# Optimization experiments

Hardware: AMD Instinct MI355X
Metric: run time of the kernel (lower is better)

## Reference

```python
import jax, jax.numpy as jnp
import numpy as np

H, W = 96, 96          # output field size
D = 32                 # window_radius
WIN = 2 * D + 1        # 65
A, B, R = 15.0, 3.0, 1
EXP = 1.0 / (1 + R)    # exponent in the stable-like covariance


def _extract_patches(noise2d):
    wi = jnp.arange(WIN)
    rows = (jnp.arange(H)[:, None, None, None] + wi[None, None, :, None])
    cols = (jnp.arange(W)[None, :, None, None] + wi[None, None, None, :])
    patches = noise2d[rows, cols]
    return patches.reshape(H * W, WIN, WIN)


def _batch_autocorrelation(theta_vec):
    x = jnp.linspace(-D, D, WIN, dtype=jnp.float32)
    Xm, Ym = jnp.meshgrid(x, x, indexing='ij')
    c = jnp.cos(theta_vec)[:, None, None]
    s = jnp.sin(theta_vec)[:, None, None]
    a_part = (Xm[None] * c + Ym[None] * s) ** 2 / (A ** 2)
    b_part = (-Xm[None] * s + Ym[None] * c) ** 2 / (B ** 2)
    return jnp.exp(-(a_part + b_part) ** EXP)


def setup_inputs() -> dict:
    key = jax.random.key(0)
    k1, k2 = jax.random.split(key)
    angle_matrix = jax.random.uniform(k1, (H, W), dtype=jnp.float32) * (2.0 * np.pi)
    noise = jax.random.normal(k2, (1, 1, H + 2 * D, W + 2 * D), dtype=jnp.float32)
    return {"angle_matrix": angle_matrix, "noise": noise}


def reference(angle_matrix, noise):
    patches = _extract_patches(noise[0, 0])
    R_stack = _batch_autocorrelation(angle_matrix.reshape(-1))
    Wf = jnp.fft.fft2(patches)
    Rf = jnp.fft.fft2(jnp.fft.fftshift(R_stack, axes=(-2, -1)))
    G = jnp.sqrt(Rf + 1e-8)                                 # complex sqrt
    v = jnp.fft.ifft2(Wf * G).real
    mean = v.mean(axis=(1, 2), keepdims=True)
    std = v.std(axis=(1, 2), keepdims=True, ddof=1)         # torch unbiased std
    v = (v - mean) / (std + 1e-6)
    return v[:, D, D].reshape(H, W)
```

## Files before the change

kernel.cpp:

```cpp
#include <hip/hip_runtime.h>
#include <math.h>

#define HH 96
#define WW 96
#define NWIN 65
#define NZ 160
#define L33 33
#define PAD 36
#define NT 256
#define KT 3
#define NG 22

__global__ __launch_bounds__(NT)
void rowdft_kernel(const float* __restrict__ noise, float2* __restrict__ rd)
{
    __shared__ float row[NZ];
    __shared__ float2 tw[NWIN];
    const int tid = threadIdx.x;
    const int r = blockIdx.x;
    if (tid < NWIN) {
        double a = 6.283185307179586 * (double)tid / 65.0;
        tw[tid] = make_float2((float)cos(a), (float)sin(a));
    }
    if (tid < NZ) row[tid] = noise[r * NZ + tid];
    __syncthreads();

    for (int t = tid; t < 96 * 9; t += NT) {
        const int px = t / 9;
        const int g = t - 9 * px;
        const int l0 = 4 * g;
        float c0[4], c1[4], s0[4], s1[4], tc2[4], aC[4], aS[4];
        #pragma unroll
        for (int j = 0; j < 4; j++) {
            float2 w = tw[l0 + j];
            c0[j] = 1.f; s0[j] = 0.f;
            c1[j] = w.x; s1[j] = w.y;
            tc2[j] = 2.f * w.x;
            aC[j] = 0.f; aS[j] = 0.f;
        }
        for (int wx = 0; wx < NWIN; ++wx) {
            float v = row[px + wx];
            #pragma unroll
            for (int j = 0; j < 4; j++) {
                aC[j] = fmaf(v, c0[j], aC[j]);
                aS[j] = fmaf(v, s0[j], aS[j]);
                float cn = fmaf(tc2[j], c1[j], -c0[j]);
                float sn = fmaf(tc2[j], s1[j], -s0[j]);
                c0[j] = c1[j]; c1[j] = cn;
                s0[j] = s1[j]; s1[j] = sn;
            }
        }
        #pragma unroll
        for (int j = 0; j < 4; j++) {
            int l = l0 + j;
            if (l < L33) rd[(px * NZ + r) * L33 + l] = make_float2(aC[j], aS[j]);
        }
    }
}

__global__ __launch_bounds__(NT)
void fftma2_kernel(const float* __restrict__ angle,
                   const float2* __restrict__ rd,
                   float* __restrict__ out)
{
    __shared__ float2 tw[NWIN];
    __shared__ alignas(16) float  RbT[NWIN][PAD];
    __shared__ alignas(16) float  Tc[L33][PAD];
    __shared__ alignas(16) float  Ts[L33][PAD];
    __shared__ alignas(16) float2 Wst[NWIN][PAD];
    __shared__ float red[4][4];

    const int tid = threadIdx.x;
    const int p  = blockIdx.x;
    const int py = p / WW;
    const int px = p - py * WW;

    if (tid < NWIN) {
        double a = 6.283185307179586 * (double)tid / 65.0;
        tw[tid] = make_float2((float)cos(a), (float)sin(a));
    }

    const float th = angle[p];
    const float cth = cosf(th), sth = sinf(th);

    for (int e = tid; e < NWIN * PAD; e += NT) {
        int y = e / PAD, x = e - PAD * y;
        float v = 0.f;
        if (x < L33) {
            float X = (float)x;
            float Y = (float)(y <= 32 ? y : y - 65);
            float u =  X * cth + Y * sth;
            float w = -X * sth + Y * cth;
            float q = fmaf(u * (1.f / 225.f), u, w * (1.f / 9.f) * w);
            v = expf(-sqrtf(q));
        }
        RbT[y][x] = v;
    }
    {
        const float2* src = rd + (px * NZ + py) * L33;
        for (int e = tid; e < NWIN * PAD; e += NT) {
            int y = e / PAD, l = e - PAD * y;
            float2 v = make_float2(0.f, 0.f);
            if (l < L33) v = src[y * L33 + l];
            Wst[y][l] = v;
        }
    }
    __syncthreads();

    for (int t = tid; t < 9 * PAD; t += NT) {
        int xg = t / PAD, l = t - PAD * xg;
        int x0 = 4 * xg;
        float aC[4] = {0,0,0,0}, aS[4] = {0,0,0,0};
        float2 wl = tw[l];
        float cm = 1.f, sm = 0.f;
        float cc = wl.x, ss = wl.y;
        float t2 = 2.f * wl.x;
        for (int y = 0; y < NWIN; ++y) {
            const float4 rv = *(const float4*)&RbT[y][x0];
            aC[0] = fmaf(rv.x, cm, aC[0]); aS[0] = fmaf(rv.x, sm, aS[0]);
            aC[1] = fmaf(rv.y, cm, aC[1]); aS[1] = fmaf(rv.y, sm, aS[1]);
            aC[2] = fmaf(rv.z, cm, aC[2]); aS[2] = fmaf(rv.z, sm, aS[2]);
            aC[3] = fmaf(rv.w, cm, aC[3]); aS[3] = fmaf(rv.w, sm, aS[3]);
            float cn = fmaf(t2, cc, -cm);
            float sn = fmaf(t2, ss, -sm);
            cm = cc; sm = ss; cc = cn; ss = sn;
        }
        #pragma unroll
        for (int j = 0; j < 4; j++) {
            int x = x0 + j;
            if (x < L33) { Tc[x][l] = aC[j]; Ts[x][l] = aS[j]; }
        }
    }
    __syncthreads();

    float accA = 0.f, accP = 0.f, accC = 0.f, accV = 0.f;
    if (tid < NG * 9) {
        const int g  = tid / 9;
        const int lg = tid - 9 * g;
        const int l0 = 4 * lg;
        const int kb = KT * g;

        float stc2[KT], sc1[KT], ss1[KT];
        #pragma unroll
        for (int d = 0; d < KT; d++) {
            int kc = kb + d; if (kc >= NWIN) kc -= NWIN;
            float2 w = tw[kc];
            sc1[d] = w.x; ss1[d] = w.y; stc2[d] = 2.f * w.x;
        }

        const float4 tc0 = *(const float4*)&Tc[0][l0];
        float ac[KT][4];
        #pragma unroll
        for (int d = 0; d < KT; d++)
            #pragma unroll
            for (int j = 0; j < 4; j++) ac[d][j] = 0.f;
        {
            float cm[KT], sm[KT], cc[KT], ss[KT];
            #pragma unroll
            for (int d = 0; d < KT; d++) {
                cm[d] = 1.f; sm[d] = 0.f;
                cc[d] = sc1[d]; ss[d] = ss1[d];
            }
            for (int x = 1; x < L33; ++x) {
                const float4 c4 = *(const float4*)&Tc[x][l0];
                const float4 s4 = *(const float4*)&Ts[x][l0];
                #pragma unroll
                for (int d = 0; d < KT; d++) {
                    float cw = cc[d], sw = ss[d];
                    ac[d][0] = fmaf(c4.x, cw, ac[d][0]); ac[d][0] = fmaf(-s4.x, sw, ac[d][0]);
                    ac[d][1] = fmaf(c4.y, cw, ac[d][1]); ac[d][1] = fmaf(-s4.y, sw, ac[d][1]);
                    ac[d][2] = fmaf(c4.z, cw, ac[d][2]); ac[d][2] = fmaf(-s4.z, sw, ac[d][2]);
                    ac[d][3] = fmaf(c4.w, cw, ac[d][3]); ac[d][3] = fmaf(-s4.w, sw, ac[d][3]);
                    float cn = fmaf(stc2[d], cw, -cm[d]);
                    float sn = fmaf(stc2[d], sw, -sm[d]);
                    cm[d] = cw; sm[d] = sw; cc[d] = cn; ss[d] = sn;
                }
            }
        }

        float Wr[KT][4], Wi[KT][4];
        #pragma unroll
        for (int d = 0; d < KT; d++)
            #pragma unroll
            for (int j = 0; j < 4; j++) { Wr[d][j] = 0.f; Wi[d][j] = 0.f; }
        {
            float cm[KT], sm[KT], cc[KT], ss[KT];
            #pragma unroll
            for (int d = 0; d < KT; d++) {
                cm[d] = 1.f; sm[d] = 0.f;
                cc[d] = sc1[d]; ss[d] = ss1[d];
            }
            for (int y = 0; y < NWIN; ++y) {
                const float4 w01 = *(const float4*)&Wst[y][l0];
                const float4 w23 = *(const float4*)&Wst[y][l0 + 2];
                #pragma unroll
                for (int d = 0; d < KT; d++) {
                    float cw = cm[d], sw = sm[d];
                    Wr[d][0] = fmaf(w01.x, cw, Wr[d][0]); Wr[d][0] = fmaf(-w01.y, sw, Wr[d][0]);
                    Wi[d][0] = fmaf(-w01.x, sw, Wi[d][0]); Wi[d][0] = fmaf(-w01.y, cw, Wi[d][0]);
                    Wr[d][1] = fmaf(w01.z, cw, Wr[d][1]); Wr[d][1] = fmaf(-w01.w, sw, Wr[d][1]);
                    Wi[d][1] = fmaf(-w01.z, sw, Wi[d][1]); Wi[d][1] = fmaf(-w01.w, cw, Wi[d][1]);
                    Wr[d][2] = fmaf(w23.x, cw, Wr[d][2]); Wr[d][2] = fmaf(-w23.y, sw, Wr[d][2]);
                    Wi[d][2] = fmaf(-w23.x, sw, Wi[d][2]); Wi[d][2] = fmaf(-w23.y, cw, Wi[d][2]);
                    Wr[d][3] = fmaf(w23.z, cw, Wr[d][3]); Wr[d][3] = fmaf(-w23.w, sw, Wr[d][3]);
                    Wi[d][3] = fmaf(-w23.z, sw, Wi[d][3]); Wi[d][3] = fmaf(-w23.w, cw, Wi[d][3]);
                    float cn = fmaf(stc2[d], cc[d], -cw);
                    float sn = fmaf(stc2[d], ss[d], -sw);
                    cm[d] = cc[d]; sm[d] = ss[d]; cc[d] = cn; ss[d] = sn;
                }
            }
        }

        #pragma unroll
        for (int d = 0; d < KT; d++) {
            const int k = kb + d;
            if (k >= NWIN) continue;
            #pragma unroll
            for (int j = 0; j < 4; j++) {
                const int l = l0 + j;
                if (l > 32) continue;
                if (l == 0 && k > 32) continue;
                float wr = Wr[d][j], wi = Wi[d][j];
                float rho = fmaf(2.f, ac[d][j], (j==0)?tc0.x:(j==1)?tc0.y:(j==2)?tc0.z:tc0.w);
                int kl = k + l; if (kl >= NWIN) kl -= NWIN;
                float2 tkl = tw[kl];
                float zr = fmaf(rho, tkl.x, 1e-8f);
                float zi = rho * tkl.y;
                float rr = sqrtf(zr * zr + zi * zi);
                float Gr = sqrtf(fmaxf(0.5f * (rr + zr), 0.f));
                float Gm = sqrtf(fmaxf(0.5f * (rr - zr), 0.f));
                float Gi = (zi < 0.f) ? -Gm : Gm;
                float Fr = wr * Gr - wi * Gi;
                float Fi = wr * Gi + wi * Gr;
                if (k == 0 && l == 0) {
                    accA += Fr * Fr + Fi * Fi;
                    accP += Fr * Fr - Fi * Fi;
                    accC += Fr;
                    accV += Fr;
                } else {
                    float Gi2 = (zi == 0.f) ? Gi : -Gi;
                    float Fr2 = wr * Gr + wi * Gi2;
                    float Fi2 = wr * Gi2 - wi * Gr;
                    accA += Fr * Fr + Fi * Fi + Fr2 * Fr2 + Fi2 * Fi2;
                    accP += 2.f * (Fr * Fr2 - Fi * Fi2);
                    int m32 = (32 * (k + l)) % NWIN;
                    float2 t32 = tw[m32];
                    accC += Fr * t32.x - Fi * t32.y + Fr2 * t32.x + Fi2 * t32.y;
                }
            }
        }
    }

    #pragma unroll
    for (int off = 32; off > 0; off >>= 1) {
        accA += __shfl_down(accA, off);
        accP += __shfl_down(accP, off);
        accC += __shfl_down(accC, off);
        accV += __shfl_down(accV, off);
    }
    int wv = tid >> 6, ln = tid & 63;
    if (ln == 0) { red[wv][0] = accA; red[wv][1] = accP; red[wv][2] = accC; red[wv][3] = accV; }
    __syncthreads();
    if (tid == 0) {
        float A  = red[0][0] + red[1][0] + red[2][0] + red[3][0];
        float P  = red[0][1] + red[1][1] + red[2][1] + red[3][1];
        float Cs = red[0][2] + red[1][2] + red[2][2] + red[3][2];
        float V  = red[0][3] + red[1][3] + red[2][3] + red[3][3];
        const float Ntot = 4225.f;
        float mean = V / Ntot;
        float E2   = (P + A) * (0.5f / Ntot);
        float cen  = Cs / Ntot;
        float var  = (E2 - Ntot * mean * mean) / (Ntot - 1.f);
        float sd   = sqrtf(fmaxf(var, 0.f));
        out[p] = (cen - mean) / (sd + 1e-6f);
    }
}

extern "C" void kernel_launch(void* const* d_in, const int* in_sizes, int n_in,
                              void* d_out, int out_size, void* d_ws, size_t ws_size,
                              hipStream_t stream)
{
    (void)in_sizes; (void)n_in; (void)out_size; (void)ws_size;
    const float* angle = (const float*)d_in[0];
    const float* noise = (const float*)d_in[1];
    float* outp = (float*)d_out;
    float2* rd = (float2*)d_ws;

    rowdft_kernel<<<dim3(NZ), dim3(NT), 0, stream>>>(noise, rd);
    fftma2_kernel<<<dim3(HH * WW), dim3(NT), 0, stream>>>(angle, rd, outp);
}
```

Before: 874.5 us.

## Exploit k/65-k twiddle symmetry to halve column DFT work and shrink block

The column-direction DFTs now compute cosine and sine partial sums separately for frequency k, then build the results for both k and 65-k from them. Only k in 0..32 (17 groups of two) is computed, which roughly halves the recurrence and FMA work in the final stage. The block size drops from 256 to 192 threads so that fewer threads sit idle. The cost is that the earlier staging and DFT loops run with fewer threads per block, and more accumulators are held in registers.

```diff
diff --git a/kernel.cpp b/kernel.cpp
--- a/kernel.cpp
+++ b/kernel.cpp
@@ -7,11 +7,10 @@
 #define NZ 160
 #define L33 33
 #define PAD 36
-#define NT 256
-#define KT 3
-#define NG 22
-
-__global__ __launch_bounds__(NT)
+#define NT1 256
+#define NT2 192
+
+__global__ __launch_bounds__(NT1)
 void rowdft_kernel(const float* __restrict__ noise, float2* __restrict__ rd)
 {
     __shared__ float row[NZ];
@@ -25,7 +24,7 @@
     if (tid < NZ) row[tid] = noise[r * NZ + tid];
     __syncthreads();
 
-    for (int t = tid; t < 96 * 9; t += NT) {
+    for (int t = tid; t < 96 * 9; t += NT1) {
         const int px = t / 9;
         const int g = t - 9 * px;
         const int l0 = 4 * g;
@@ -58,7 +57,7 @@
     }
 }
 
-__global__ __launch_bounds__(NT)
+__global__ __launch_bounds__(NT2)
 void fftma2_kernel(const float* __restrict__ angle,
                    const float2* __restrict__ rd,
                    float* __restrict__ out)
@@ -68,7 +67,7 @@
     __shared__ alignas(16) float  Tc[L33][PAD];
     __shared__ alignas(16) float  Ts[L33][PAD];
     __shared__ alignas(16) float2 Wst[NWIN][PAD];
-    __shared__ float red[4][4];
+    __shared__ float red[3][4];
 
     const int tid = threadIdx.x;
     const int p  = blockIdx.x;
@@ -83,7 +82,7 @@
     const float th = angle[p];
     const float cth = cosf(th), sth = sinf(th);
 
-    for (int e = tid; e < NWIN * PAD; e += NT) {
+    for (int e = tid; e < NWIN * PAD; e += NT2) {
         int y = e / PAD, x = e - PAD * y;
         float v = 0.f;
         if (x < L33) {
@@ -98,7 +97,7 @@
     }
     {
         const float2* src = rd + (px * NZ + py) * L33;
-        for (int e = tid; e < NWIN * PAD; e += NT) {
+        for (int e = tid; e < NWIN * PAD; e += NT2) {
             int y = e / PAD, l = e - PAD * y;
             float2 v = make_float2(0.f, 0.f);
             if (l < L33) v = src[y * L33 + l];
@@ -107,7 +106,7 @@
     }
     __syncthreads();
 
-    for (int t = tid; t < 9 * PAD; t += NT) {
+    for (int t = tid; t < 9 * PAD; t += NT2) {
         int xg = t / PAD, l = t - PAD * xg;
         int x0 = 4 * xg;
         float aC[4] = {0,0,0,0}, aS[4] = {0,0,0,0};
@@ -134,118 +133,123 @@
     __syncthreads();
 
     float accA = 0.f, accP = 0.f, accC = 0.f, accV = 0.f;
-    if (tid < NG * 9) {
+    if (tid < 17 * 9) {
         const int g  = tid / 9;
         const int lg = tid - 9 * g;
         const int l0 = 4 * lg;
-        const int kb = KT * g;
-
-        float stc2[KT], sc1[KT], ss1[KT];
-        #pragma unroll
-        for (int d = 0; d < KT; d++) {
-            int kc = kb + d; if (kc >= NWIN) kc -= NWIN;
-            float2 w = tw[kc];
-            sc1[d] = w.x; ss1[d] = w.y; stc2[d] = 2.f * w.x;
-        }
-
+
+        float sc1[2], ss1[2], st2[2];
+        #pragma unroll
+        for (int d = 0; d < 2; d++) {
+            float2 w = tw[2 * g + d];
+            sc1[d] = w.x; ss1[d] = w.y; st2[d] = 2.f * w.x;
+        }
         const float4 tc0 = *(const float4*)&Tc[0][l0];
-        float ac[KT][4];
-        #pragma unroll
-        for (int d = 0; d < KT; d++)
-            #pragma unroll
-            for (int j = 0; j < 4; j++) ac[d][j] = 0.f;
+
+        float P[2][4], Q[2][4];
+        #pragma unroll
+        for (int d = 0; d < 2; d++)
+            #pragma unroll
+            for (int j = 0; j < 4; j++) { P[d][j] = 0.f; Q[d][j] = 0.f; }
         {
-            float cm[KT], sm[KT], cc[KT], ss[KT];
-            #pragma unroll
-            for (int d = 0; d < KT; d++) {
-                cm[d] = 1.f; sm[d] = 0.f;
-                cc[d] = sc1[d]; ss[d] = ss1[d];
-            }
+            float cm[2] = {1.f, 1.f}, sm[2] = {0.f, 0.f};
+            float cc[2] = {sc1[0], sc1[1]}, ss[2] = {ss1[0], ss1[1]};
             for (int x = 1; x < L33; ++x) {
                 const float4 c4 = *(const float4*)&Tc[x][l0];
                 const float4 s4 = *(const float4*)&Ts[x][l0];
                 #pragma unroll
-                for (int d = 0; d < KT; d++) {
+                for (int d = 0; d < 2; d++) {
                     float cw = cc[d], sw = ss[d];
-                    ac[d][0] = fmaf(c4.x, cw, ac[d][0]); ac[d][0] = fmaf(-s4.x, sw, ac[d][0]);
-                    ac[d][1] = fmaf(c4.y, cw, ac[d][1]); ac[d][1] = fmaf(-s4.y, sw, ac[d][1]);
-                    ac[d][2] = fmaf(c4.z, cw, ac[d][2]); ac[d][2] = fmaf(-s4.z, sw, ac[d][2]);
-                    ac[d][3] = fmaf(c4.w, cw, ac[d][3]); ac[d][3] = fmaf(-s4.w, sw, ac[d][3]);
-                    float cn = fmaf(stc2[d], cw, -cm[d]);
-                    float sn = fmaf(stc2[d], sw, -sm[d]);
+                    P[d][0] = fmaf(c4.x, cw, P[d][0]); Q[d][0] = fmaf(s4.x, sw, Q[d][0]);
+                    P[d][1] = fmaf(c4.y, cw, P[d][1]); Q[d][1] = fmaf(s4.y, sw, Q[d][1]);
+                    P[d][2] = fmaf(c4.z, cw, P[d][2]); Q[d][2] = fmaf(s4.z, sw, Q[d][2]);
+                    P[d][3] = fmaf(c4.w, cw, P[d][3]); Q[d][3] = fmaf(s4.w, sw, Q[d][3]);
+                    float cn = fmaf(st2[d], cw, -cm[d]);
+                    float sn = fmaf(st2[d], sw, -sm[d]);
                     cm[d] = cw; sm[d] = sw; cc[d] = cn; ss[d] = sn;
                 }
             }
         }
-
-        float Wr[KT][4], Wi[KT][4];
-        #pragma unroll
-        for (int d = 0; d < KT; d++)
-            #pragma unroll
-            for (int j = 0; j < 4; j++) { Wr[d][j] = 0.f; Wi[d][j] = 0.f; }
+        float rfm[2][4], rfp[2][4];
+        #pragma unroll
+        for (int d = 0; d < 2; d++)
+            #pragma unroll
+            for (int j = 0; j < 4; j++) {
+                float t0 = (j == 0) ? tc0.x : (j == 1) ? tc0.y : (j == 2) ? tc0.z : tc0.w;
+                rfm[d][j] = fmaf(2.f, P[d][j] - Q[d][j], t0);
+                rfp[d][j] = fmaf(2.f, P[d][j] + Q[d][j], t0);
+            }
+
+        float A[2][4], B[2][4], C[2][4], D[2][4];
+        #pragma unroll
+        for (int d = 0; d < 2; d++)
+            #pragma unroll
+            for (int j = 0; j < 4; j++) { A[d][j] = 0.f; B[d][j] = 0.f; C[d][j] = 0.f; D[d][j] = 0.f; }
         {
-            float cm[KT], sm[KT], cc[KT], ss[KT];
-            #pragma unroll
-            for (int d = 0; d < KT; d++) {
-                cm[d] = 1.f; sm[d] = 0.f;
-                cc[d] = sc1[d]; ss[d] = ss1[d];
-            }
+            float cm[2] = {1.f, 1.f}, sm[2] = {0.f, 0.f};
+            float cc[2] = {sc1[0], sc1[1]}, ss[2] = {ss1[0], ss1[1]};
             for (int y = 0; y < NWIN; ++y) {
                 const float4 w01 = *(const float4*)&Wst[y][l0];
                 const float4 w23 = *(const float4*)&Wst[y][l0 + 2];
                 #pragma unroll
-                for (int d = 0; d < KT; d++) {
+                for (int d = 0; d < 2; d++) {
                     float cw = cm[d], sw = sm[d];
-                    Wr[d][0] = fmaf(w01.x, cw, Wr[d][0]); Wr[d][0] = fmaf(-w01.y, sw, Wr[d][0]);
-                    Wi[d][0] = fmaf(-w01.x, sw, Wi[d][0]); Wi[d][0] = fmaf(-w01.y, cw, Wi[d][0]);
-                    Wr[d][1] = fmaf(w01.z, cw, Wr[d][1]); Wr[d][1] = fmaf(-w01.w, sw, Wr[d][1]);
-                    Wi[d][1] = fmaf(-w01.z, sw, Wi[d][1]); Wi[d][1] = fmaf(-w01.w, cw, Wi[d][1]);
-                    Wr[d][2] = fmaf(w23.x, cw, Wr[d][2]); Wr[d][2] = fmaf(-w23.y, sw, Wr[d][2]);
-                    Wi[d][2] = fmaf(-w23.x, sw, Wi[d][2]); Wi[d][2] = fmaf(-w23.y, cw, Wi[d][2]);
-                    Wr[d][3] = fmaf(w23.z, cw, Wr[d][3]); Wr[d][3] = fmaf(-w23.w, sw, Wr[d][3]);
-                    Wi[d][3] = fmaf(-w23.z, sw, Wi[d][3]); Wi[d][3] = fmaf(-w23.w, cw, Wi[d][3]);
-                    float cn = fmaf(stc2[d], cc[d], -cw);
-                    float sn = fmaf(stc2[d], ss[d], -sw);
+                    A[d][0] = fmaf(w01.x, cw, A[d][0]); B[d][0] = fmaf(w01.y, sw, B[d][0]);
+                    C[d][0] = fmaf(w01.x, sw, C[d][0]); D[d][0] = fmaf(w01.y, cw, D[d][0]);
+                    A[d][1] = fmaf(w01.z, cw, A[d][1]); B[d][1] = fmaf(w01.w, sw, B[d][1]);
+                    C[d][1] = fmaf(w01.z, sw, C[d][1]); D[d][1] = fmaf(w01.w, cw, D[d][1]);
+                    A[d][2] = fmaf(w23.x, cw, A[d][2]); B[d][2] = fmaf(w23.y, sw, B[d][2]);
+                    C[d][2] = fmaf(w23.x, sw, C[d][2]); D[d][2] = fmaf(w23.y, cw, D[d][2]);
+                    A[d][3] = fmaf(w23.z, cw, A[d][3]); B[d][3] = fmaf(w23.w, sw, B[d][3]);
+                    C[d][3] = fmaf(w23.z, sw, C[d][3]); D[d][3] = fmaf(w23.w, cw, D[d][3]);
+                    float cn = fmaf(st2[d], cc[d], -cw);
+                    float sn = fmaf(st2[d], ss[d], -sw);
                     cm[d] = cc[d]; sm[d] = ss[d]; cc[d] = cn; ss[d] = sn;
                 }
             }
         }
 
         #pragma unroll
-        for (int d = 0; d < KT; d++) {
-            const int k = kb + d;
-            if (k >= NWIN) continue;
-            #pragma unroll
-            for (int j = 0; j < 4; j++) {
-                const int l = l0 + j;
-                if (l > 32) continue;
-                if (l == 0 && k > 32) continue;
-                float wr = Wr[d][j], wi = Wi[d][j];
-                float rho = fmaf(2.f, ac[d][j], (j==0)?tc0.x:(j==1)?tc0.y:(j==2)?tc0.z:tc0.w);
-                int kl = k + l; if (kl >= NWIN) kl -= NWIN;
-                float2 tkl = tw[kl];
-                float zr = fmaf(rho, tkl.x, 1e-8f);
-                float zi = rho * tkl.y;
-                float rr = sqrtf(zr * zr + zi * zi);
-                float Gr = sqrtf(fmaxf(0.5f * (rr + zr), 0.f));
-                float Gm = sqrtf(fmaxf(0.5f * (rr - zr), 0.f));
-                float Gi = (zi < 0.f) ? -Gm : Gm;
-                float Fr = wr * Gr - wi * Gi;
-                float Fi = wr * Gi + wi * Gr;
-                if (k == 0 && l == 0) {
-                    accA += Fr * Fr + Fi * Fi;
-                    accP += Fr * Fr - Fi * Fi;
-                    accC += Fr;
-                    accV += Fr;
-                } else {
-                    float Gi2 = (zi == 0.f) ? Gi : -Gi;
-                    float Fr2 = wr * Gr + wi * Gi2;
-                    float Fi2 = wr * Gi2 - wi * Gr;
-                    accA += Fr * Fr + Fi * Fi + Fr2 * Fr2 + Fi2 * Fi2;
-                    accP += 2.f * (Fr * Fr2 - Fi * Fi2);
-                    int m32 = (32 * (k + l)) % NWIN;
-                    float2 t32 = tw[m32];
-                    accC += Fr * t32.x - Fi * t32.y + Fr2 * t32.x + Fi2 * t32.y;
+        for (int d = 0; d < 2; d++) {
+            const int kp = 2 * g + d;
+            if (kp > 32) continue;
+            #pragma unroll
+            for (int e = 0; e < 2; e++) {
+                if (e == 1 && kp == 0) continue;
+                const int kk = e ? (65 - kp) : kp;
+                #pragma unroll
+                for (int j = 0; j < 4; j++) {
+                    const int l = l0 + j;
+                    if (l > 32) continue;
+                    if (l == 0 && kk > 32) continue;
+                    float wr  = e ? (A[d][j] + B[d][j]) : (A[d][j] - B[d][j]);
+                    float wi  = e ? (C[d][j] - D[d][j]) : (-(C[d][j] + D[d][j]));
+                    float rho = e ? rfp[d][j] : rfm[d][j];
+                    int kl = kk + l; if (kl >= NWIN) kl -= NWIN;
+                    float2 tkl = tw[kl];
+                    float zr = fmaf(rho, tkl.x, 1e-8f);
+                    float zi = rho * tkl.y;
+                    float rr = sqrtf(zr * zr + zi * zi);
+                    float Gr = sqrtf(fmaxf(0.5f * (rr + zr), 0.f));
+                    float Gm = sqrtf(fmaxf(0.5f * (rr - zr), 0.f));
+                    float Gi = (zi < 0.f) ? -Gm : Gm;
+                    float Fr = wr * Gr - wi * Gi;
+                    float Fi = wr * Gi + wi * Gr;
+                    if (kk == 0 && l == 0) {
+                        accA += Fr * Fr + Fi * Fi;
+                        accP += Fr * Fr - Fi * Fi;
+                        accC += Fr;
+                        accV += Fr;
+                    } else {
+                        float Gi2 = (zi == 0.f) ? Gi : -Gi;
+                        float Fr2 = wr * Gr + wi * Gi2;
+                        float Fi2 = wr * Gi2 - wi * Gr;
+                        accA += Fr * Fr + Fi * Fi + Fr2 * Fr2 + Fi2 * Fi2;
+                        accP += 2.f * (Fr * Fr2 - Fi * Fi2);
+                        int m32 = (32 * (kk + l)) % NWIN;
+                        float2 t32 = tw[m32];
+                        accC += Fr * t32.x - Fi * t32.y + Fr2 * t32.x + Fi2 * t32.y;
+                    }
                 }
             }
         }
@@ -262,14 +266,14 @@
     if (ln == 0) { red[wv][0] = accA; red[wv][1] = accP; red[wv][2] = accC; red[wv][3] = accV; }
     __syncthreads();
     if (tid == 0) {
-        float A  = red[0][0] + red[1][0] + red[2][0] + red[3][0];
-        float P  = red[0][1] + red[1][1] + red[2][1] + red[3][1];
-        float Cs = red[0][2] + red[1][2] + red[2][2] + red[3][2];
-        float V  = red[0][3] + red[1][3] + red[2][3] + red[3][3];
+        float Asum = red[0][0] + red[1][0] + red[2][0];
+        float Psum = red[0][1] + red[1][1] + red[2][1];
+        float Csum = red[0][2] + red[1][2] + red[2][2];
+        float Vsum = red[0][3] + red[1][3] + red[2][3];
         const float Ntot = 4225.f;
-        float mean = V / Ntot;
-        float E2   = (P + A) * (0.5f / Ntot);
-        float cen  = Cs / Ntot;
+        float mean = Vsum / Ntot;
+        float E2   = (Psum + Asum) * (0.5f / Ntot);
+        float cen  = Csum / Ntot;
         float var  = (E2 - Ntot * mean * mean) / (Ntot - 1.f);
         float sd   = sqrtf(fmaxf(var, 0.f));
         out[p] = (cen - mean) / (sd + 1e-6f);
@@ -286,6 +290,6 @@
     float* outp = (float*)d_out;
     float2* rd = (float2*)d_ws;
 
-    rowdft_kernel<<<dim3(NZ), dim3(NT), 0, stream>>>(noise, rd);
-    fftma2_kernel<<<dim3(HH * WW), dim3(NT), 0, stream>>>(angle, rd, outp);
+    rowdft_kernel<<<dim3(NZ), dim3(NT1), 0, stream>>>(noise, rd);
+    fftma2_kernel<<<dim3(HH * WW), dim3(NT2), 0, stream>>>(angle, rd, outp);
 }
```

Measured after the change: 765.4 us. 1.14x faster.
